# Kernel optimization log

Hardware: AMD Instinct MI355X
Metric: run time of the kernel (lower is better)

The kernel has to match this reference:

```python
import jax, jax.numpy as jnp
import numpy as np

# bitsandbytes NF4 codebook (16 levels)
NF4 = jnp.array([-1.0, -0.6961928009986877, -0.5250730514526367, -0.39491748809814453,
                 -0.28444138169288635, -0.18477343022823334, -0.09105003625154495, 0.0,
                 0.07958029955625534, 0.16093020141124725, 0.24611230194568634,
                 0.33791524171829224, 0.44070982933044434, 0.5626170039176941,
                 0.7229568362236023, 1.0], dtype=jnp.float32)
BLOCK = 64  # NF4 quantization blocksize
HD, M, TOKENS = 4096, 11008, 512


def dequant_nf4(codes, absmax, out_f, in_f):
    # codes: int [out_f, in_f] in [0,16); absmax: float [out_f*in_f/BLOCK]
    w = NF4[codes.reshape(-1, BLOCK)] * absmax[:, None]
    return w.reshape(out_f, in_f)


def setup_inputs() -> dict:
    key = jax.random.key(0)
    ks = jax.random.split(key, 7)
    x = jax.random.normal(ks[0], (TOKENS, HD), dtype=jnp.float32)
    gate_codes = jax.random.randint(ks[1], (M, HD), 0, 16, dtype=jnp.int32)
    up_codes = jax.random.randint(ks[2], (M, HD), 0, 16, dtype=jnp.int32)
    down_codes = jax.random.randint(ks[3], (HD, M), 0, 16, dtype=jnp.int32)
    n_blk = (M * HD) // BLOCK
    gate_absmax = jax.random.uniform(ks[4], (n_blk,), dtype=jnp.float32) * 0.02 + 1e-3
    up_absmax = jax.random.uniform(ks[5], (n_blk,), dtype=jnp.float32) * 0.02 + 1e-3
    down_absmax = jax.random.uniform(ks[6], (n_blk,), dtype=jnp.float32) * 0.02 + 1e-3
    return {"x": x, "gate_codes": gate_codes, "gate_absmax": gate_absmax,
            "up_codes": up_codes, "up_absmax": up_absmax,
            "down_codes": down_codes, "down_absmax": down_absmax}


def reference(x, gate_codes, gate_absmax, up_codes, up_absmax, down_codes, down_absmax):
    # Dequantize NF4 weights on the fly, then SwiGLU MLP:
    # down( silu(gate(x)) * up(x) )
    Wg = dequant_nf4(gate_codes, gate_absmax, M, HD)   # [m, hd]
    Wu = dequant_nf4(up_codes, up_absmax, M, HD)       # [m, hd]
    Wd = dequant_nf4(down_codes, down_absmax, HD, M)   # [hd, m]
    g = x @ Wg.T                                       # [tokens, m]
    u = x @ Wu.T                                       # [tokens, m]
    h = jax.nn.silu(g) * u                             # [tokens, m]
    return h @ Wd.T                                    # [tokens, hd]
```

## Files before the change

kernel.cpp:

```cpp
#include <hip/hip_runtime.h>
#include <hip/hip_bf16.h>
#include <cstdint>
#include <cstddef>

#define TOKENS 512

using float4v = __attribute__((ext_vector_type(4))) float;
using short8  = __attribute__((ext_vector_type(8))) short;

__constant__ float NF4TAB[16] = {
  -1.0f, -0.6961928009986877f, -0.5250730514526367f, -0.39491748809814453f,
  -0.28444138169288635f, -0.18477343022823334f, -0.09105003625154495f, 0.0f,
  0.07958029955625534f, 0.16093020141124725f, 0.24611230194568634f,
  0.33791524171829224f, 0.44070982933044434f, 0.5626170039176941f,
  0.7229568362236023f, 1.0f };

__device__ __forceinline__ unsigned short f2bf(float f) {
  unsigned u = __float_as_uint(f);
  u += 0x7fffu + ((u >> 16) & 1u);
  return (unsigned short)(u >> 16);
}
__device__ __forceinline__ float bf2f(unsigned short b) {
  return __uint_as_float(((unsigned)b) << 16);
}

__device__ __forceinline__ void async16(const void* g, void* l) {
  __builtin_amdgcn_global_load_lds(
      (const __attribute__((address_space(1))) void*)g,
      (__attribute__((address_space(3))) void*)l, 16, 0, 0);
}

template <int EPI>
__global__ __launch_bounds__(256) void gemm_nf4(
    const unsigned short* __restrict__ A,
    const int* __restrict__ codes,
    const float* __restrict__ absmax,
    float* __restrict__ outF,
    unsigned short* __restrict__ outB,
    const unsigned short* __restrict__ gIn,
    int N, int K, int Kc, int Mtiles, int Ntiles)
{
  __shared__ unsigned short Abuf[256 * 64];
  __shared__ unsigned short Bbuf[64 * 72];
  __shared__ float tab[16];

  const int tid  = threadIdx.x;
  const int lane = tid & 63;
  const int wave = tid >> 6;

  if (tid < 16) tab[tid] = NF4TAB[tid];

  const int bid = blockIdx.x;
  const int mt  = bid % Mtiles;
  const int r1  = bid / Mtiles;
  const int nt  = r1 % Ntiles;
  const int ks  = r1 / Ntiles;

  const int row0 = mt * 256;
  const int col0 = nt * 64;
  const int k0   = ks * Kc;
  const int nk   = Kc >> 6;

  const int arow = lane >> 3;
  const int achk = (lane & 7) ^ arow;
  const unsigned short* aSrc0 =
      A + (size_t)(row0 + wave * 8 + arow) * K + k0 + achk * 8;

  const int bn = tid >> 2;
  const int bq = tid & 3;
  const int* cSrc = codes + (size_t)(col0 + bn) * K + k0;
  const float* amSrc = absmax + (size_t)(col0 + bn) * (K >> 6) + (k0 >> 6);

  float4v acc[4][4];
  {
    float4v z = {0.f, 0.f, 0.f, 0.f};
    #pragma unroll
    for (int i = 0; i < 4; ++i)
      #pragma unroll
      for (int j = 0; j < 4; ++j) acc[i][j] = z;
  }

  __syncthreads();

  for (int kt = 0; kt < nk; ++kt) {
    #pragma unroll
    for (int j = 0; j < 8; ++j) {
      async16(aSrc0 + (size_t)j * 32 * K + kt * 64,
              &Abuf[(j * 4 + wave) * 512]);
    }
    const float am = amSrc[kt];
    #pragma unroll
    for (int i = 0; i < 4; ++i) {
      int4 c4 = ((const int4*)(cSrc + kt * 64))[i * 4 + bq];
      ushort4 w;
      w.x = f2bf(tab[c4.x] * am);
      w.y = f2bf(tab[c4.y] * am);
      w.z = f2bf(tab[c4.z] * am);
      w.w = f2bf(tab[c4.w] * am);
      *(ushort4*)&Bbuf[bn * 72 + i * 16 + bq * 4] = w;
    }
    __syncthreads();

    #pragma unroll
    for (int kk = 0; kk < 2; ++kk) {
      short8 af[4], bfr[4];
      #pragma unroll
      for (int i = 0; i < 4; ++i) {
        const int row_l = wave * 64 + i * 16 + (lane & 15);
        const int gl    = kk * 4 + (lane >> 4);
        const int phys  = gl ^ (lane & 7);
        af[i] = *(const short8*)&Abuf[row_l * 64 + phys * 8];
      }
      #pragma unroll
      for (int j = 0; j < 4; ++j) {
        const int n_l = j * 16 + (lane & 15);
        bfr[j] = *(const short8*)&Bbuf[n_l * 72 + kk * 32 + (lane >> 4) * 8];
      }
      #pragma unroll
      for (int i = 0; i < 4; ++i)
        #pragma unroll
        for (int j = 0; j < 4; ++j)
          acc[i][j] = __builtin_amdgcn_mfma_f32_16x16x32_bf16(af[i], bfr[j], acc[i][j], 0, 0, 0);
    }
    __syncthreads();
  }

  const int ccol  = col0 + (lane & 15);
  const int crow0 = row0 + wave * 64 + ((lane >> 4) << 2);
  #pragma unroll
  for (int i = 0; i < 4; ++i) {
    #pragma unroll
    for (int j = 0; j < 4; ++j) {
      #pragma unroll
      for (int r = 0; r < 4; ++r) {
        const size_t idx = (size_t)(crow0 + i * 16 + r) * N + (ccol + j * 16);
        if (EPI == 2) {
          atomicAdd(&outF[idx], acc[i][j][r]);
        } else if (EPI == 0) {
          outB[idx] = f2bf(acc[i][j][r]);
        } else {
          const float gv = bf2f(gIn[idx]);
          const float s  = gv / (1.f + __expf(-gv));
          outB[idx] = f2bf(s * acc[i][j][r]);
        }
      }
    }
  }
}

__global__ void cast_bf16_kernel(const float* __restrict__ x,
                                 unsigned short* __restrict__ xb, int n4) {
  int i = blockIdx.x * blockDim.x + threadIdx.x;
  if (i < n4) {
    float4 v = ((const float4*)x)[i];
    ushort4 o;
    o.x = f2bf(v.x); o.y = f2bf(v.y); o.z = f2bf(v.z); o.w = f2bf(v.w);
    ((ushort4*)xb)[i] = o;
  }
}

extern "C" void kernel_launch(void* const* d_in, const int* in_sizes, int n_in,
                              void* d_out, int out_size, void* d_ws, size_t ws_size,
                              hipStream_t stream)
{
  (void)in_sizes; (void)n_in; (void)ws_size;
  const float* x            = (const float*)d_in[0];
  const int*   gate_codes   = (const int*)d_in[1];
  const float* gate_absmax  = (const float*)d_in[2];
  const int*   up_codes     = (const int*)d_in[3];
  const float* up_absmax    = (const float*)d_in[4];
  const int*   down_codes   = (const int*)d_in[5];
  const float* down_absmax  = (const float*)d_in[6];
  float* out = (float*)d_out;

  unsigned short* xb = (unsigned short*)d_ws;
  unsigned short* g  = xb + (size_t)512 * 4096;
  unsigned short* h  = g  + (size_t)512 * 11008;

  hipMemsetAsync(d_out, 0, (size_t)out_size * sizeof(float), stream);

  cast_bf16_kernel<<<2048, 256, 0, stream>>>(x, xb, (512 * 4096) / 4);

  gemm_nf4<0><<<344, 256, 0, stream>>>(xb, gate_codes, gate_absmax,
                                       nullptr, g, nullptr,
                                       11008, 4096, 4096, 2, 172);
  gemm_nf4<1><<<344, 256, 0, stream>>>(xb, up_codes, up_absmax,
                                       nullptr, h, g,
                                       11008, 4096, 4096, 2, 172);
  gemm_nf4<2><<<512, 256, 0, stream>>>(h, down_codes, down_absmax,
                                       out, nullptr, nullptr,
                                       4096, 11008, 2752, 2, 64);
}
```

Baseline: 761.8 us.

## Double-buffer LDS tiles, shrink M tile to 128, and use a 2x2 wave layout

Adds double-buffered LDS for the A and dequantized B tiles and prefetches the next tile's codes into registers, so global loads and dequantization overlap the MFMA work on the current tile. It halves the M tile from 256 to 128 rows, arranges the four waves as 2x2 over M and N, and doubles the grid sizes. It also sets a 3-blocks-per-CU launch bound for occupancy. The risk is that each NF4 code tile is now dequantized twice, once per M tile, which doubles code-read and dequant traffic.

```diff
diff --git a/kernel.cpp b/kernel.cpp
--- a/kernel.cpp
+++ b/kernel.cpp
@@ -3,7 +3,6 @@
 #include <cstdint>
 #include <cstddef>
 
-#define TOKENS 512
 
 using float4v = __attribute__((ext_vector_type(4))) float;
 using short8  = __attribute__((ext_vector_type(8))) short;
@@ -23,7 +22,6 @@
 __device__ __forceinline__ float bf2f(unsigned short b) {
   return __uint_as_float(((unsigned)b) << 16);
 }
-
 __device__ __forceinline__ void async16(const void* g, void* l) {
   __builtin_amdgcn_global_load_lds(
       (const __attribute__((address_space(1))) void*)g,
@@ -31,7 +29,7 @@
 }
 
 template <int EPI>
-__global__ __launch_bounds__(256) void gemm_nf4(
+__global__ __launch_bounds__(256, 3) void gemm_nf4(
     const unsigned short* __restrict__ A,
     const int* __restrict__ codes,
     const float* __restrict__ absmax,
@@ -40,13 +38,15 @@
     const unsigned short* __restrict__ gIn,
     int N, int K, int Kc, int Mtiles, int Ntiles)
 {
-  __shared__ unsigned short Abuf[256 * 64];
-  __shared__ unsigned short Bbuf[64 * 72];
+  __shared__ unsigned short Abuf[2][128 * 64];
+  __shared__ unsigned short Bbuf[2][64 * 72];
   __shared__ float tab[16];
 
   const int tid  = threadIdx.x;
   const int lane = tid & 63;
   const int wave = tid >> 6;
+  const int wm   = wave & 1;
+  const int wn   = wave >> 1;
 
   if (tid < 16) tab[tid] = NF4TAB[tid];
 
@@ -56,84 +56,97 @@
   const int nt  = r1 % Ntiles;
   const int ks  = r1 / Ntiles;
 
-  const int row0 = mt * 256;
+  const int row0 = mt * 128;
   const int col0 = nt * 64;
   const int k0   = ks * Kc;
   const int nk   = Kc >> 6;
 
   const int arow = lane >> 3;
   const int achk = (lane & 7) ^ arow;
-  const unsigned short* aSrc0 =
-      A + (size_t)(row0 + wave * 8 + arow) * K + k0 + achk * 8;
+  const unsigned short* aSrc =
+      A + (size_t)(row0 + wave * 32 + arow) * K + k0 + achk * 8;
 
   const int bn = tid >> 2;
   const int bq = tid & 3;
   const int* cSrc = codes + (size_t)(col0 + bn) * K + k0;
   const float* amSrc = absmax + (size_t)(col0 + bn) * (K >> 6) + (k0 >> 6);
 
-  float4v acc[4][4];
+  float4v acc[4][2];
   {
     float4v z = {0.f, 0.f, 0.f, 0.f};
     #pragma unroll
     for (int i = 0; i < 4; ++i)
       #pragma unroll
-      for (int j = 0; j < 4; ++j) acc[i][j] = z;
-  }
+      for (int j = 0; j < 2; ++j) acc[i][j] = z;
+  }
+
+#define STAGEA(kt, buf)                                                         \
+  { _Pragma("unroll")                                                           \
+    for (int j = 0; j < 4; ++j)                                                 \
+      async16(aSrc + (size_t)j * 8 * K + (size_t)(kt) * 64,                     \
+              &Abuf[buf][(wave * 32 + j * 8) * 64]); }
+
+#define LOADC(kt)                                                               \
+  { const int4* p = (const int4*)(cSrc + (kt) * 64);                            \
+    cr[0] = p[bq]; cr[1] = p[4 + bq]; cr[2] = p[8 + bq]; cr[3] = p[12 + bq];    \
+    am = amSrc[kt]; }
+
+#define DEQB(buf)                                                               \
+  { _Pragma("unroll")                                                           \
+    for (int i = 0; i < 4; ++i) {                                               \
+      ushort4 w;                                                                \
+      w.x = f2bf(tab[cr[i].x] * am); w.y = f2bf(tab[cr[i].y] * am);             \
+      w.z = f2bf(tab[cr[i].z] * am); w.w = f2bf(tab[cr[i].w] * am);             \
+      *(ushort4*)&Bbuf[buf][bn * 72 + i * 16 + bq * 4] = w; } }
 
   __syncthreads();
 
+  int4 cr[4]; float am;
+  STAGEA(0, 0);
+  LOADC(0);
+  DEQB(0);
+  if (nk > 1) LOADC(1);
+  __syncthreads();
+
   for (int kt = 0; kt < nk; ++kt) {
-    #pragma unroll
-    for (int j = 0; j < 8; ++j) {
-      async16(aSrc0 + (size_t)j * 32 * K + kt * 64,
-              &Abuf[(j * 4 + wave) * 512]);
+    const int p = kt & 1, np = p ^ 1;
+    if (kt + 1 < nk) {
+      STAGEA(kt + 1, np);
+      DEQB(np);
+      if (kt + 2 < nk) LOADC(kt + 2);
     }
-    const float am = amSrc[kt];
-    #pragma unroll
-    for (int i = 0; i < 4; ++i) {
-      int4 c4 = ((const int4*)(cSrc + kt * 64))[i * 4 + bq];
-      ushort4 w;
-      w.x = f2bf(tab[c4.x] * am);
-      w.y = f2bf(tab[c4.y] * am);
-      w.z = f2bf(tab[c4.z] * am);
-      w.w = f2bf(tab[c4.w] * am);
-      *(ushort4*)&Bbuf[bn * 72 + i * 16 + bq * 4] = w;
-    }
-    __syncthreads();
-
     #pragma unroll
     for (int kk = 0; kk < 2; ++kk) {
-      short8 af[4], bfr[4];
+      short8 af[4], bfr[2];
       #pragma unroll
       for (int i = 0; i < 4; ++i) {
-        const int row_l = wave * 64 + i * 16 + (lane & 15);
-        const int gl    = kk * 4 + (lane >> 4);
-        const int phys  = gl ^ (lane & 7);
-        af[i] = *(const short8*)&Abuf[row_l * 64 + phys * 8];
+        const int row_l = wm * 64 + i * 16 + (lane & 15);
+        const int phys  = (kk * 4 + (lane >> 4)) ^ (row_l & 7);
+        af[i] = *(const short8*)&Abuf[p][row_l * 64 + phys * 8];
       }
       #pragma unroll
-      for (int j = 0; j < 4; ++j) {
-        const int n_l = j * 16 + (lane & 15);
-        bfr[j] = *(const short8*)&Bbuf[n_l * 72 + kk * 32 + (lane >> 4) * 8];
+      for (int j = 0; j < 2; ++j) {
+        const int n_l = wn * 32 + j * 16 + (lane & 15);
+        bfr[j] = *(const short8*)&Bbuf[p][n_l * 72 + kk * 32 + (lane >> 4) * 8];
       }
       #pragma unroll
       for (int i = 0; i < 4; ++i)
         #pragma unroll
-        for (int j = 0; j < 4; ++j)
+        for (int j = 0; j < 2; ++j)
           acc[i][j] = __builtin_amdgcn_mfma_f32_16x16x32_bf16(af[i], bfr[j], acc[i][j], 0, 0, 0);
     }
     __syncthreads();
   }
 
-  const int ccol  = col0 + (lane & 15);
-  const int crow0 = row0 + wave * 64 + ((lane >> 4) << 2);
+  const int ccol0 = col0 + wn * 32 + (lane & 15);
+  const int crow0 = row0 + wm * 64 + ((lane >> 4) << 2);
   #pragma unroll
   for (int i = 0; i < 4; ++i) {
     #pragma unroll
-    for (int j = 0; j < 4; ++j) {
+    for (int j = 0; j < 2; ++j) {
       #pragma unroll
       for (int r = 0; r < 4; ++r) {
-        const size_t idx = (size_t)(crow0 + i * 16 + r) * N + (ccol + j * 16);
+        const size_t idx = (size_t)(crow0 + i * 16 + r) * N + (ccol0 + j * 16);
         if (EPI == 2) {
           atomicAdd(&outF[idx], acc[i][j][r]);
         } else if (EPI == 0) {
@@ -146,6 +159,9 @@
       }
     }
   }
+#undef STAGEA
+#undef LOADC
+#undef DEQB
 }
 
 __global__ void cast_bf16_kernel(const float* __restrict__ x,
@@ -181,13 +197,13 @@
 
   cast_bf16_kernel<<<2048, 256, 0, stream>>>(x, xb, (512 * 4096) / 4);
 
-  gemm_nf4<0><<<344, 256, 0, stream>>>(xb, gate_codes, gate_absmax,
+  gemm_nf4<0><<<688, 256, 0, stream>>>(xb, gate_codes, gate_absmax,
                                        nullptr, g, nullptr,
-                                       11008, 4096, 4096, 2, 172);
-  gemm_nf4<1><<<344, 256, 0, stream>>>(xb, up_codes, up_absmax,
+                                       11008, 4096, 4096, 4, 172);
+  gemm_nf4<1><<<688, 256, 0, stream>>>(xb, up_codes, up_absmax,
                                        nullptr, h, g,
-                                       11008, 4096, 4096, 2, 172);
-  gemm_nf4<2><<<512, 256, 0, stream>>>(h, down_codes, down_absmax,
-                                       out, nullptr, nullptr,
-                                       4096, 11008, 2752, 2, 64);
-}
+                                       11008, 4096, 4096, 4, 172);
+  gemm_nf4<2><<<1024, 256, 0, stream>>>(h, down_codes, down_absmax,
+                                        out, nullptr, nullptr,
+                                        4096, 11008, 2752, 4, 64);
+}
```

After: 875.1 us. 14.9% more time.
